# Performance work log

Hardware: AMD Instinct MI355X
Metric: run time of the kernel (lower is better)

The kernel has to match this reference:

```python
import jax, jax.numpy as jnp
import numpy as np

N, H, E, K, C, M = 4096, 512, 512, 64, 128, 4  # tokens, hidden, embed, categories, children/cat, max_num_children
IN = E + H  # LSTMCell input size


def setup_inputs() -> dict:
    key = jax.random.key(0)
    ks = jax.random.split(key, 12)
    s = 0.05
    return {
        "et": jax.random.normal(ks[0], (N, H), jnp.float32),
        "x": jax.random.normal(ks[1], (N, IN), jnp.float32),
        "h": jax.random.normal(ks[2], (N, H), jnp.float32),
        "c": jax.random.normal(ks[3], (N, H), jnp.float32),
        "cat": jax.random.randint(ks[4], (N,), 0, K, jnp.int32),
        "ci": jax.random.randint(ks[5], (N,), 0, M, jnp.int32),
        # per-category prediction Linear(hidden_size -> |children(category)|)
        "W_lin": jax.random.normal(ks[6], (K, C, H), jnp.float32) * s,
        "b_lin": jax.random.normal(ks[7], (K, C), jnp.float32) * s,
        # per-child-index LSTMCell(embedding+hidden -> hidden), torch gate order i,f,g,o
        "W_ih": jax.random.normal(ks[8], (M, 4 * H, IN), jnp.float32) * s,
        "W_hh": jax.random.normal(ks[9], (M, 4 * H, H), jnp.float32) * s,
        "b_ih": jax.random.normal(ks[10], (M, 4 * H), jnp.float32) * s,
        "b_hh": jax.random.normal(ks[11], (M, 4 * H), jnp.float32) * s,
    }


def reference(et, x, h, c, cat, ci, W_lin, b_lin, W_ih, W_hh, b_ih, b_hh):
    # get_log_odds: route each token to its category's Linear (gather weights, per-token matvec)
    Wg = W_lin[cat]                                   # [N, C, H]
    log_odds = jnp.einsum('nh,nch->nc', et, Wg) + b_lin[cat]  # [N, C]

    # get_next: LSTMCell selected by child_index. Only M=4 cells, so compute all
    # cells' gates densely (efficient GEMMs) and select with a one-hot mix.
    gates_all = (jnp.einsum('ni,kgi->nkg', x, W_ih)
                 + jnp.einsum('nh,kgh->nkg', h, W_hh)
                 + (b_ih + b_hh)[None])               # [N, M, 4H]
    sel = jax.nn.one_hot(ci, M, dtype=gates_all.dtype)  # [N, M]
    gates = jnp.einsum('nkg,nk->ng', gates_all, sel)     # [N, 4H]
    i_, f_, g_, o_ = jnp.split(gates, 4, axis=-1)
    c2 = jax.nn.sigmoid(f_) * c + jax.nn.sigmoid(i_) * jnp.tanh(g_)
    h2 = jax.nn.sigmoid(o_) * jnp.tanh(c2)
    return log_odds, h2, c2
```

## Files before the change

kernel.cpp:

```cpp
#include <hip/hip_runtime.h>
#include <hip/hip_bf16.h>
#include <stdint.h>

#define NTOK 4096
#define HID  512
#define INSZ 1024
#define KIN  1536
#define KCAT 64
#define CCH  128
#define MCELL 4
#define G4H  2048
#define SLOTS 4992

typedef unsigned short u16;
typedef __bf16 bf16x8 __attribute__((ext_vector_type(8)));
typedef float  f32x4  __attribute__((ext_vector_type(4)));

__device__ __forceinline__ u16 f2bf(float f) {
    unsigned u = __float_as_uint(f);
    u += 0x7fffu + ((u >> 16) & 1u);
    return (u16)(u >> 16);
}
__device__ __forceinline__ float bf2f(u16 v) {
    return __uint_as_float(((unsigned)v) << 16);
}
__device__ __forceinline__ void store_bf8(u16* p, float4 a, float4 b) {
    ushort4 r0, r1;
    r0.x = f2bf(a.x); r0.y = f2bf(a.y); r0.z = f2bf(a.z); r0.w = f2bf(a.w);
    r1.x = f2bf(b.x); r1.y = f2bf(b.y); r1.z = f2bf(b.z); r1.w = f2bf(b.w);
    *reinterpret_cast<ushort4*>(p) = r0;
    *reinterpret_cast<ushort4*>(p + 4) = r1;
}
__device__ __forceinline__ void gl16(const u16* g, u16* l) {
    __builtin_amdgcn_global_load_lds((const __attribute__((address_space(1))) void*)g,
                                     (__attribute__((address_space(3))) void*)l, 16, 0, 0);
}

#define CH_W  (8192 * 192)
#define CH_L  (8192 * 64)
#define CH_A  (4097 * 192)
#define CH_TOT (CH_W + CH_L + CH_A)
#define PK_BLOCKS 2048

__global__ __launch_bounds__(256) void fat_pack(
    const float* __restrict__ x, const float* __restrict__ h,
    const float* __restrict__ Wih, const float* __restrict__ Whh,
    const float* __restrict__ W_lin,
    const int* __restrict__ ci, const int* __restrict__ cat,
    int* __restrict__ meta, int* __restrict__ perm_ci, int* __restrict__ perm_cat,
    u16* __restrict__ A_tok, u16* __restrict__ Wb, u16* __restrict__ Wlin)
{
    if (blockIdx.x == 0) {
        __shared__ int cnt_ci[MCELL], cur_ci[MCELL];
        __shared__ int cnt_cat[KCAT], cur_cat[KCAT];
        __shared__ int scan_cat[KCAT];
        int tid = threadIdx.x;
        if (tid < MCELL) cnt_ci[tid] = 0;
        if (tid < KCAT)  cnt_cat[tid] = 0;
        __syncthreads();
        for (int t = tid; t < NTOK; t += 256) {
            atomicAdd(&cnt_ci[ci[t]], 1);
            atomicAdd(&cnt_cat[cat[t]], 1);
        }
        __syncthreads();
        for (int i = tid; i < 128; i += 256) meta[136 + i] = -1;
        if (tid < MCELL) {
            int off = 0;
            for (int i = 0; i < tid; ++i) off += (cnt_ci[i] + 191) / 192 * 192;
            int p = (cnt_ci[tid] + 191) / 192 * 192;
            meta[tid] = p; meta[4 + tid] = off; cur_ci[tid] = off;
        }
        if (tid < KCAT) scan_cat[tid] = (cnt_cat[tid] + 63) & ~63;
        __syncthreads();
        for (int d = 1; d < KCAT; d <<= 1) {
            int v = 0;
            if (tid < KCAT && tid >= d) v = scan_cat[tid - d];
            __syncthreads();
            if (tid < KCAT) scan_cat[tid] += v;
            __syncthreads();
        }
        if (tid < KCAT) {
            int p = (cnt_cat[tid] + 63) & ~63;
            int off = scan_cat[tid] - p;
            meta[8 + tid] = p; meta[72 + tid] = off; cur_cat[tid] = off;
            for (int i = 0; i < p / 64; ++i) meta[136 + off / 64 + i] = tid;
        }
        __syncthreads();
        for (int i = tid; i < SLOTS; i += 256) perm_ci[i] = -1;
        for (int i = tid; i < 8192; i += 256) perm_cat[i] = -1;
        __syncthreads();
        for (int t = tid; t < NTOK; t += 256) {
            perm_ci[atomicAdd(&cur_ci[ci[t]], 1)] = t;
            perm_cat[atomicAdd(&cur_cat[cat[t]], 1)] = t;
        }
        return;
    }
    for (int i = (blockIdx.x - 1) * 256 + threadIdx.x; i < CH_TOT; i += (PK_BLOCKS - 1) * 256) {
        if (i < CH_W) {
            int row = i / 192, cc = i - row * 192;
            int m = row >> 11, j = row & 2047;
            int srow = (j & 3) * HID + (j >> 2);
            int c = cc * 8;
            const float* src = (c < INSZ) ? (Wih + ((size_t)m * G4H + srow) * INSZ + c)
                                          : (Whh + ((size_t)m * G4H + srow) * HID + (c - INSZ));
            store_bf8(Wb + (size_t)row * KIN + c,
                      *(const float4*)src, *(const float4*)(src + 4));
        } else if (i < CH_W + CH_L) {
            int i2 = i - CH_W;
            int row = i2 >> 6, cc = i2 & 63;
            const float* src = W_lin + (size_t)row * HID + cc * 8;
            store_bf8(Wlin + (size_t)row * HID + cc * 8,
                      *(const float4*)src, *(const float4*)(src + 4));
        } else {
            int i3 = i - (CH_W + CH_L);
            int row = i3 / 192, cc = i3 - row * 192;
            int c = cc * 8;
            u16* dst = A_tok + (size_t)row * KIN + c;
            if (row == NTOK) {
                *reinterpret_cast<int4*>(dst) = make_int4(0, 0, 0, 0);
            } else {
                const float* src = (c < INSZ) ? (x + (size_t)row * INSZ + c)
                                              : (h + (size_t)row * HID + (c - INSZ));
                store_bf8(dst, *(const float4*)src, *(const float4*)(src + 4));
            }
        }
    }
}

__global__ __launch_bounds__(256, 3) void mega_gemm(
    const u16* __restrict__ A_tok,
    const u16* __restrict__ Wb,
    const u16* __restrict__ Wlin,
    const float* __restrict__ et,
    const float* __restrict__ b_lin,
    const float* __restrict__ c,
    const float* __restrict__ b_ih,
    const float* __restrict__ b_hh,
    const int* __restrict__ meta,
    const int* __restrict__ perm_ci,
    const int* __restrict__ perm_cat,
    float* __restrict__ out)
{
    __shared__ __align__(16) u16 S[20480];
    __shared__ int sperm[192];

    int tid = threadIdx.x;
    int lane = tid & 63, wave = tid >> 6;
    int qd = lane >> 4, l15 = lane & 15;
    int rsw = l15 & 7;

    int id = blockIdx.x;
    if (id < 1408) {
        int g = id & 63;
        int rt = id >> 6;
        int m = g >> 4, ct = g & 15;
        int pcnt = meta[m];
        if (rt * 192 >= pcnt) return;
        int row0 = meta[4 + m] + rt * 192;

        if (tid < 192) sperm[tid] = perm_ci[row0 + tid];
        __syncthreads();

        const u16* gA[6]; const u16* gB[4];
        u16* lA[6]; u16* lB[4];
        #pragma unroll
        for (int j = 0; j < 6; ++j) {
            int q = j * 256 + tid;
            int row = q >> 3, kc = (q & 7) ^ (row & 7);
            int t = sperm[row];
            gA[j] = A_tok + (size_t)(t >= 0 ? t : NTOK) * KIN + kc * 8;
            lA[j] = &S[q * 8];
        }
        #pragma unroll
        for (int j = 0; j < 4; ++j) {
            int q = j * 256 + tid;
            int row = q >> 3, kc = (q & 7) ^ (row & 7);
            gB[j] = Wb + ((size_t)m * G4H + ct * 128 + row) * KIN + kc * 8;
            lB[j] = &S[12288 + q * 8];
        }

        int wm = wave >> 1, wn = wave & 1;

        f32x4 acc[6][4];
        #pragma unroll
        for (int i = 0; i < 6; ++i)
            #pragma unroll
            for (int j = 0; j < 4; ++j)
                acc[i][j] = (f32x4){0.f, 0.f, 0.f, 0.f};

        for (int ks = 0; ks < KIN / 64; ++ks) {
            #pragma unroll
            for (int j = 0; j < 6; ++j) { gl16(gA[j], lA[j]); gA[j] += 64; }
            #pragma unroll
            for (int j = 0; j < 4; ++j) { gl16(gB[j], lB[j]); gB[j] += 64; }
            __syncthreads();
            #pragma unroll
            for (int ks2 = 0; ks2 < 2; ++ks2) {
                int ch = (ks2 * 4 + qd) ^ rsw;
                bf16x8 fb[4];
                #pragma unroll
                for (int tj = 0; tj < 4; ++tj) {
                    int row = wn * 64 + tj * 16 + l15;
                    fb[tj] = *reinterpret_cast<const bf16x8*>(&S[12288 + row * 64 + ch * 8]);
                }
                #pragma unroll
                for (int ti = 0; ti < 6; ++ti) {
                    int row = wm * 96 + ti * 16 + l15;
                    bf16x8 fa = *reinterpret_cast<const bf16x8*>(&S[row * 64 + ch * 8]);
                    #pragma unroll
                    for (int tj = 0; tj < 4; ++tj)
                        acc[ti][tj] = __builtin_amdgcn_mfma_f32_16x16x32_bf16(fa, fb[tj], acc[ti][tj], 0, 0, 0);
                }
            }
            __syncthreads();
        }

        int gt = l15 & 3;
        float bias[4];
        #pragma unroll
        for (int tj = 0; tj < 4; ++tj) {
            int u = ct * 32 + wn * 16 + tj * 4 + (l15 >> 2);
            bias[tj] = b_ih[m * G4H + gt * HID + u] + b_hh[m * G4H + gt * HID + u];
        }
        int b0 = lane & 1, b1 = lane & 2;
        const size_t o_h2 = (size_t)NTOK * CCH;
        const size_t o_c2 = o_h2 + (size_t)NTOK * HID;
        #pragma unroll
        for (int ti = 0; ti < 6; ++ti) {
            int t = sperm[wm * 96 + ti * 16 + qd * 4 + (lane & 3)];
            #pragma unroll
            for (int tj = 0; tj < 4; ++tj) {
                float v0 = acc[ti][tj][0] + bias[tj];
                float v1 = acc[ti][tj][1] + bias[tj];
                float v2 = acc[ti][tj][2] + bias[tj];
                float v3 = acc[ti][tj][3] + bias[tj];
                float tmp;
                tmp = __shfl_xor(b0 ? v0 : v1, 1); if (b0) v0 = tmp; else v1 = tmp;
                tmp = __shfl_xor(b0 ? v2 : v3, 1); if (b0) v2 = tmp; else v3 = tmp;
                tmp = __shfl_xor(b1 ? v0 : v2, 2); if (b1) v0 = tmp; else v2 = tmp;
                tmp = __shfl_xor(b1 ? v1 : v3, 2); if (b1) v1 = tmp; else v3 = tmp;
                if (t >= 0) {
                    int u = ct * 32 + wn * 16 + tj * 4 + (l15 >> 2);
                    float si = 1.f / (1.f + __expf(-v0));
                    float sf = 1.f / (1.f + __expf(-v1));
                    float tg = tanhf(v2);
                    float so = 1.f / (1.f + __expf(-v3));
                    float cold = c[(size_t)t * HID + u];
                    float c2 = sf * cold + si * tg;
                    float h2 = so * tanhf(c2);
                    out[o_h2 + (size_t)t * HID + u] = h2;
                    out[o_c2 + (size_t)t * HID + u] = c2;
                }
            }
        }
    } else {
        u16* As = S;
        u16* Bs = S + 8192;
        int rtl = id - 1408;
        int k = meta[136 + rtl];
        if (k < 0) return;
        int r0 = rtl * 64;

        if (tid < 64) sperm[tid] = perm_cat[r0 + tid];
        __syncthreads();

        int rb = tid >> 3;
        int kc = (tid & 7) ^ (rb & 7);

        const u16* gW[4]; u16* lW[4];
        #pragma unroll
        for (int i = 0; i < 4; ++i) {
            gW[i] = Wlin + ((size_t)k * CCH + i * 32 + rb) * HID + kc * 8;
            lW[i] = As + (i * 256 + wave * 64) * 8;
        }
        int ar = tid >> 2;
        int acp = tid & 3;
        int at = sperm[ar];
        const float* asrc = (at >= 0) ? (et + (size_t)at * HID) : nullptr;

        f32x4 acc[4][2];
        #pragma unroll
        for (int i = 0; i < 4; ++i) {
            acc[i][0] = (f32x4){0.f, 0.f, 0.f, 0.f};
            acc[i][1] = (f32x4){0.f, 0.f, 0.f, 0.f};
        }

        for (int kk = 0; kk < HID; kk += 64) {
            #pragma unroll
            for (int i = 0; i < 4; ++i) { gl16(gW[i], lW[i]); gW[i] += 64; }
            #pragma unroll
            for (int j = 0; j < 2; ++j) {
                int dch = acp * 2 + j;
                int sch = dch ^ (ar & 7);
                u16* dst = &Bs[ar * 64 + dch * 8];
                if (asrc) {
                    const float* s = asrc + kk + sch * 8;
                    store_bf8(dst, *(const float4*)s, *(const float4*)(s + 4));
                } else {
                    *reinterpret_cast<int4*>(dst) = make_int4(0, 0, 0, 0);
                }
            }
            __syncthreads();
            #pragma unroll
            for (int ks2 = 0; ks2 < 2; ++ks2) {
                int ch = (ks2 * 4 + qd) ^ rsw;
                bf16x8 fa[4], fb[2];
                #pragma unroll
                for (int ti = 0; ti < 4; ++ti)
                    fa[ti] = *reinterpret_cast<const bf16x8*>(&Bs[(ti * 16 + l15) * 64 + ch * 8]);
                #pragma unroll
                for (int tj = 0; tj < 2; ++tj)
                    fb[tj] = *reinterpret_cast<const bf16x8*>(&As[(wave * 32 + tj * 16 + l15) * 64 + ch * 8]);
                #pragma unroll
                for (int ti = 0; ti < 4; ++ti)
                    #pragma unroll
                    for (int tj = 0; tj < 2; ++tj)
                        acc[ti][tj] = __builtin_amdgcn_mfma_f32_16x16x32_bf16(fa[ti], fb[tj], acc[ti][tj], 0, 0, 0);
            }
            __syncthreads();
        }

        #pragma unroll
        for (int ti = 0; ti < 4; ++ti) {
            #pragma unroll
            for (int tj = 0; tj < 2; ++tj) {
                int n = wave * 32 + tj * 16 + l15;
                float bias = b_lin[k * CCH + n];
                #pragma unroll
                for (int rr = 0; rr < 4; ++rr) {
                    int row = ti * 16 + qd * 4 + rr;
                    int t = sperm[row];
                    if (t >= 0)
                        out[(size_t)t * CCH + n] = acc[ti][tj][rr] + bias;
                }
            }
        }
    }
}

extern "C" void kernel_launch(void* const* d_in, const int* in_sizes, int n_in,
                              void* d_out, int out_size, void* d_ws, size_t ws_size,
                              hipStream_t stream) {
    const float* et    = (const float*)d_in[0];
    const float* x     = (const float*)d_in[1];
    const float* h     = (const float*)d_in[2];
    const float* c     = (const float*)d_in[3];
    const int*   cat   = (const int*)d_in[4];
    const int*   ci    = (const int*)d_in[5];
    const float* W_lin = (const float*)d_in[6];
    const float* b_lin = (const float*)d_in[7];
    const float* W_ih  = (const float*)d_in[8];
    const float* W_hh  = (const float*)d_in[9];
    const float* b_ih  = (const float*)d_in[10];
    const float* b_hh  = (const float*)d_in[11];
    float* out = (float*)d_out;

    char* ws = (char*)d_ws;
    int* meta     = (int*)ws;
    int* perm_ci  = (int*)(ws + 2048);
    int* perm_cat = (int*)(ws + 22528);
    u16* A_tok    = (u16*)(ws + 55296);
    u16* Wb       = (u16*)(ws + 12641280);
    u16* Wlin     = (u16*)(ws + 37807104);

    fat_pack<<<PK_BLOCKS, 256, 0, stream>>>(x, h, W_ih, W_hh, W_lin, ci, cat,
                                            meta, perm_ci, perm_cat, A_tok, Wb, Wlin);

    mega_gemm<<<1408 + 128, 256, 0, stream>>>(A_tok, Wb, Wlin, et, b_lin, c,
                                              b_ih, b_hh, meta, perm_ci, perm_cat, out);
}
```

Before: 220.7 us.

## Widen LSTM GEMM tiles to 512 threads and convert W_lin inline

```diff
diff --git a/kernel.cpp b/kernel.cpp
--- a/kernel.cpp
+++ b/kernel.cpp
@@ -37,18 +37,16 @@
 }
 
 #define CH_W  (8192 * 192)
-#define CH_L  (8192 * 64)
 #define CH_A  (4097 * 192)
-#define CH_TOT (CH_W + CH_L + CH_A)
+#define CH_TOT (CH_W + CH_A)
 #define PK_BLOCKS 2048
 
 __global__ __launch_bounds__(256) void fat_pack(
     const float* __restrict__ x, const float* __restrict__ h,
     const float* __restrict__ Wih, const float* __restrict__ Whh,
-    const float* __restrict__ W_lin,
     const int* __restrict__ ci, const int* __restrict__ cat,
     int* __restrict__ meta, int* __restrict__ perm_ci, int* __restrict__ perm_cat,
-    u16* __restrict__ A_tok, u16* __restrict__ Wb, u16* __restrict__ Wlin)
+    u16* __restrict__ A_tok, u16* __restrict__ Wb)
 {
     if (blockIdx.x == 0) {
         __shared__ int cnt_ci[MCELL], cur_ci[MCELL];
@@ -105,14 +103,8 @@
                                           : (Whh + ((size_t)m * G4H + srow) * HID + (c - INSZ));
             store_bf8(Wb + (size_t)row * KIN + c,
                       *(const float4*)src, *(const float4*)(src + 4));
-        } else if (i < CH_W + CH_L) {
-            int i2 = i - CH_W;
-            int row = i2 >> 6, cc = i2 & 63;
-            const float* src = W_lin + (size_t)row * HID + cc * 8;
-            store_bf8(Wlin + (size_t)row * HID + cc * 8,
-                      *(const float4*)src, *(const float4*)(src + 4));
         } else {
-            int i3 = i - (CH_W + CH_L);
+            int i3 = i - CH_W;
             int row = i3 / 192, cc = i3 - row * 192;
             int c = cc * 8;
             u16* dst = A_tok + (size_t)row * KIN + c;
@@ -127,10 +119,10 @@
     }
 }
 
-__global__ __launch_bounds__(256, 3) void mega_gemm(
+__global__ __launch_bounds__(512, 2) void mega_gemm(
     const u16* __restrict__ A_tok,
     const u16* __restrict__ Wb,
-    const u16* __restrict__ Wlin,
+    const float* __restrict__ W_lin,
     const float* __restrict__ et,
     const float* __restrict__ b_lin,
     const float* __restrict__ c,
@@ -141,19 +133,18 @@
     const int* __restrict__ perm_cat,
     float* __restrict__ out)
 {
-    __shared__ __align__(16) u16 S[20480];
+    __shared__ __align__(16) u16 S[28672];
     __shared__ int sperm[192];
 
     int tid = threadIdx.x;
-    int lane = tid & 63, wave = tid >> 6;
+    int lane = tid & 63;
     int qd = lane >> 4, l15 = lane & 15;
     int rsw = l15 & 7;
 
     int id = blockIdx.x;
-    if (id < 1408) {
-        int g = id & 63;
-        int rt = id >> 6;
-        int m = g >> 4, ct = g & 15;
+    if (id < 704) {
+        int g = id & 31, rt = id >> 5;
+        int m = g >> 3, ct = g & 7;
         int pcnt = meta[m];
         if (rt * 192 >= pcnt) return;
         int row0 = meta[4 + m] + rt * 192;
@@ -161,25 +152,26 @@
         if (tid < 192) sperm[tid] = perm_ci[row0 + tid];
         __syncthreads();
 
-        const u16* gA[6]; const u16* gB[4];
-        u16* lA[6]; u16* lB[4];
-        #pragma unroll
-        for (int j = 0; j < 6; ++j) {
-            int q = j * 256 + tid;
+        const u16* gA[3]; u16* lA[3];
+        #pragma unroll
+        for (int j = 0; j < 3; ++j) {
+            int q = j * 512 + tid;
             int row = q >> 3, kc = (q & 7) ^ (row & 7);
             int t = sperm[row];
             gA[j] = A_tok + (size_t)(t >= 0 ? t : NTOK) * KIN + kc * 8;
             lA[j] = &S[q * 8];
         }
+        const u16* gB[4]; u16* lB[4];
         #pragma unroll
         for (int j = 0; j < 4; ++j) {
-            int q = j * 256 + tid;
+            int q = j * 512 + tid;
             int row = q >> 3, kc = (q & 7) ^ (row & 7);
-            gB[j] = Wb + ((size_t)m * G4H + ct * 128 + row) * KIN + kc * 8;
+            gB[j] = Wb + ((size_t)m * G4H + ct * 256 + row) * KIN + kc * 8;
             lB[j] = &S[12288 + q * 8];
         }
 
-        int wm = wave >> 1, wn = wave & 1;
+        int wave = tid >> 6;
+        int wm = wave >> 2, wn = wave & 3;
 
         f32x4 acc[6][4];
         #pragma unroll
@@ -190,7 +182,7 @@
 
         for (int ks = 0; ks < KIN / 64; ++ks) {
             #pragma unroll
-            for (int j = 0; j < 6; ++j) { gl16(gA[j], lA[j]); gA[j] += 64; }
+            for (int j = 0; j < 3; ++j) { gl16(gA[j], lA[j]); gA[j] += 64; }
             #pragma unroll
             for (int j = 0; j < 4; ++j) { gl16(gB[j], lB[j]); gB[j] += 64; }
             __syncthreads();
@@ -219,7 +211,7 @@
         float bias[4];
         #pragma unroll
         for (int tj = 0; tj < 4; ++tj) {
-            int u = ct * 32 + wn * 16 + tj * 4 + (l15 >> 2);
+            int u = ct * 64 + wn * 16 + tj * 4 + (l15 >> 2);
             bias[tj] = b_ih[m * G4H + gt * HID + u] + b_hh[m * G4H + gt * HID + u];
         }
         int b0 = lane & 1, b1 = lane & 2;
@@ -240,7 +232,7 @@
                 tmp = __shfl_xor(b1 ? v0 : v2, 2); if (b1) v0 = tmp; else v2 = tmp;
                 tmp = __shfl_xor(b1 ? v1 : v3, 2); if (b1) v1 = tmp; else v3 = tmp;
                 if (t >= 0) {
-                    int u = ct * 32 + wn * 16 + tj * 4 + (l15 >> 2);
+                    int u = ct * 64 + wn * 16 + tj * 4 + (l15 >> 2);
                     float si = 1.f / (1.f + __expf(-v0));
                     float sf = 1.f / (1.f + __expf(-v1));
                     float tg = tanhf(v2);
@@ -254,28 +246,34 @@
             }
         }
     } else {
-        u16* As = S;
-        u16* Bs = S + 8192;
-        int rtl = id - 1408;
+        int half = tid >> 8;
+        int tid2 = tid & 255;
+        int wave2 = tid2 >> 6;
+        u16* As = S + half * 12288;
+        u16* Bs = As + 8192;
+        int* sp = sperm + half * 64;
+
+        int rtl = (id - 704) * 2 + half;
         int k = meta[136 + rtl];
-        if (k < 0) return;
+        int valid = (k >= 0);
+        if (!valid) k = 0;
         int r0 = rtl * 64;
 
-        if (tid < 64) sperm[tid] = perm_cat[r0 + tid];
-        __syncthreads();
-
-        int rb = tid >> 3;
-        int kc = (tid & 7) ^ (rb & 7);
-
-        const u16* gW[4]; u16* lW[4];
+        if (tid2 < 64) sp[tid2] = valid ? perm_cat[r0 + tid2] : -1;
+        __syncthreads();
+
+        int rb = tid2 >> 3;
+        int wkc = (tid2 & 7) ^ (rb & 7);
+
+        const float* wsrc[4]; u16* wdst[4];
         #pragma unroll
         for (int i = 0; i < 4; ++i) {
-            gW[i] = Wlin + ((size_t)k * CCH + i * 32 + rb) * HID + kc * 8;
-            lW[i] = As + (i * 256 + wave * 64) * 8;
-        }
-        int ar = tid >> 2;
-        int acp = tid & 3;
-        int at = sperm[ar];
+            wsrc[i] = W_lin + ((size_t)k * CCH + i * 32 + rb) * HID + wkc * 8;
+            wdst[i] = As + ((size_t)i * 256 + tid2) * 8;
+        }
+        int ar = tid2 >> 2;
+        int acp = tid2 & 3;
+        int at = sp[ar];
         const float* asrc = (at >= 0) ? (et + (size_t)at * HID) : nullptr;
 
         f32x4 acc[4][2];
@@ -287,7 +285,10 @@
 
         for (int kk = 0; kk < HID; kk += 64) {
             #pragma unroll
-            for (int i = 0; i < 4; ++i) { gl16(gW[i], lW[i]); gW[i] += 64; }
+            for (int i = 0; i < 4; ++i) {
+                const float* s = wsrc[i] + kk;
+                store_bf8(wdst[i], *(const float4*)s, *(const float4*)(s + 4));
+            }
             #pragma unroll
             for (int j = 0; j < 2; ++j) {
                 int dch = acp * 2 + j;
@@ -310,7 +311,7 @@
                     fa[ti] = *reinterpret_cast<const bf16x8*>(&Bs[(ti * 16 + l15) * 64 + ch * 8]);
                 #pragma unroll
                 for (int tj = 0; tj < 2; ++tj)
-                    fb[tj] = *reinterpret_cast<const bf16x8*>(&As[(wave * 32 + tj * 16 + l15) * 64 + ch * 8]);
+                    fb[tj] = *reinterpret_cast<const bf16x8*>(&As[(wave2 * 32 + tj * 16 + l15) * 64 + ch * 8]);
                 #pragma unroll
                 for (int ti = 0; ti < 4; ++ti)
                     #pragma unroll
@@ -324,12 +325,12 @@
         for (int ti = 0; ti < 4; ++ti) {
             #pragma unroll
             for (int tj = 0; tj < 2; ++tj) {
-                int n = wave * 32 + tj * 16 + l15;
+                int n = wave2 * 32 + tj * 16 + l15;
                 float bias = b_lin[k * CCH + n];
                 #pragma unroll
                 for (int rr = 0; rr < 4; ++rr) {
                     int row = ti * 16 + qd * 4 + rr;
-                    int t = sperm[row];
+                    int t = sp[row];
                     if (t >= 0)
                         out[(size_t)t * CCH + n] = acc[ti][tj][rr] + bias;
                 }
@@ -361,11 +362,10 @@
     int* perm_cat = (int*)(ws + 22528);
     u16* A_tok    = (u16*)(ws + 55296);
     u16* Wb       = (u16*)(ws + 12641280);
-    u16* Wlin     = (u16*)(ws + 37807104);
-
-    fat_pack<<<PK_BLOCKS, 256, 0, stream>>>(x, h, W_ih, W_hh, W_lin, ci, cat,
-                                            meta, perm_ci, perm_cat, A_tok, Wb, Wlin);
-
-    mega_gemm<<<1408 + 128, 256, 0, stream>>>(A_tok, Wb, Wlin, et, b_lin, c,
-                                              b_ih, b_hh, meta, perm_ci, perm_cat, out);
-}
+
+    fat_pack<<<PK_BLOCKS, 256, 0, stream>>>(x, h, W_ih, W_hh, ci, cat,
+                                            meta, perm_ci, perm_cat, A_tok, Wb);
+
+    mega_gemm<<<704 + 64, 512, 0, stream>>>(A_tok, Wb, W_lin, et, b_lin, c,
+                                            b_ih, b_hh, meta, perm_ci, perm_cat, out);
+}
```

Result: no change. 221.5 us (+0.4%).

## Shrink LSTM GEMM tiles to 128 rows, convert W_lin in-kernel, fast activations

Applied to the files above, without the earlier changes.

```diff
diff --git a/kernel.cpp b/kernel.cpp
--- a/kernel.cpp
+++ b/kernel.cpp
@@ -10,7 +10,7 @@
 #define CCH  128
 #define MCELL 4
 #define G4H  2048
-#define SLOTS 4992
+#define SLOTS 4608
 
 typedef unsigned short u16;
 typedef __bf16 bf16x8 __attribute__((ext_vector_type(8)));
@@ -35,20 +35,25 @@
     __builtin_amdgcn_global_load_lds((const __attribute__((address_space(1))) void*)g,
                                      (__attribute__((address_space(3))) void*)l, 16, 0, 0);
 }
+__device__ __forceinline__ float fsig(float x) {
+    return __builtin_amdgcn_rcpf(1.f + __expf(-x));
+}
+__device__ __forceinline__ float ftanh(float x) {
+    float e2 = __expf(fminf(2.f * x, 20.f));
+    return (e2 - 1.f) * __builtin_amdgcn_rcpf(e2 + 1.f);
+}
 
 #define CH_W  (8192 * 192)
-#define CH_L  (8192 * 64)
 #define CH_A  (4097 * 192)
-#define CH_TOT (CH_W + CH_L + CH_A)
+#define CH_TOT (CH_W + CH_A)
 #define PK_BLOCKS 2048
 
 __global__ __launch_bounds__(256) void fat_pack(
     const float* __restrict__ x, const float* __restrict__ h,
     const float* __restrict__ Wih, const float* __restrict__ Whh,
-    const float* __restrict__ W_lin,
     const int* __restrict__ ci, const int* __restrict__ cat,
     int* __restrict__ meta, int* __restrict__ perm_ci, int* __restrict__ perm_cat,
-    u16* __restrict__ A_tok, u16* __restrict__ Wb, u16* __restrict__ Wlin)
+    u16* __restrict__ A_tok, u16* __restrict__ Wb)
 {
     if (blockIdx.x == 0) {
         __shared__ int cnt_ci[MCELL], cur_ci[MCELL];
@@ -66,8 +71,8 @@
         for (int i = tid; i < 128; i += 256) meta[136 + i] = -1;
         if (tid < MCELL) {
             int off = 0;
-            for (int i = 0; i < tid; ++i) off += (cnt_ci[i] + 191) / 192 * 192;
-            int p = (cnt_ci[tid] + 191) / 192 * 192;
+            for (int i = 0; i < tid; ++i) off += (cnt_ci[i] + 127) & ~127;
+            int p = (cnt_ci[tid] + 127) & ~127;
             meta[tid] = p; meta[4 + tid] = off; cur_ci[tid] = off;
         }
         if (tid < KCAT) scan_cat[tid] = (cnt_cat[tid] + 63) & ~63;
@@ -105,14 +110,8 @@
                                           : (Whh + ((size_t)m * G4H + srow) * HID + (c - INSZ));
             store_bf8(Wb + (size_t)row * KIN + c,
                       *(const float4*)src, *(const float4*)(src + 4));
-        } else if (i < CH_W + CH_L) {
-            int i2 = i - CH_W;
-            int row = i2 >> 6, cc = i2 & 63;
-            const float* src = W_lin + (size_t)row * HID + cc * 8;
-            store_bf8(Wlin + (size_t)row * HID + cc * 8,
-                      *(const float4*)src, *(const float4*)(src + 4));
         } else {
-            int i3 = i - (CH_W + CH_L);
+            int i3 = i - CH_W;
             int row = i3 / 192, cc = i3 - row * 192;
             int c = cc * 8;
             u16* dst = A_tok + (size_t)row * KIN + c;
@@ -127,10 +126,10 @@
     }
 }
 
-__global__ __launch_bounds__(256, 3) void mega_gemm(
+__global__ __launch_bounds__(256, 4) void mega_gemm(
     const u16* __restrict__ A_tok,
     const u16* __restrict__ Wb,
-    const u16* __restrict__ Wlin,
+    const float* __restrict__ W_lin,
     const float* __restrict__ et,
     const float* __restrict__ b_lin,
     const float* __restrict__ c,
@@ -141,8 +140,7 @@
     const int* __restrict__ perm_cat,
     float* __restrict__ out)
 {
-    __shared__ __align__(16) u16 S[20480];
-    __shared__ int sperm[192];
+    __shared__ __align__(16) u16 S[16384];
 
     int tid = threadIdx.x;
     int lane = tid & 63, wave = tid >> 6;
@@ -150,49 +148,43 @@
     int rsw = l15 & 7;
 
     int id = blockIdx.x;
-    if (id < 1408) {
+    if (id < 2048) {
         int g = id & 63;
         int rt = id >> 6;
         int m = g >> 4, ct = g & 15;
         int pcnt = meta[m];
-        if (rt * 192 >= pcnt) return;
-        int row0 = meta[4 + m] + rt * 192;
-
-        if (tid < 192) sperm[tid] = perm_ci[row0 + tid];
-        __syncthreads();
-
-        const u16* gA[6]; const u16* gB[4];
-        u16* lA[6]; u16* lB[4];
-        #pragma unroll
-        for (int j = 0; j < 6; ++j) {
-            int q = j * 256 + tid;
-            int row = q >> 3, kc = (q & 7) ^ (row & 7);
-            int t = sperm[row];
-            gA[j] = A_tok + (size_t)(t >= 0 ? t : NTOK) * KIN + kc * 8;
-            lA[j] = &S[q * 8];
-        }
+        if (rt * 128 >= pcnt) return;
+        int row0 = meta[4 + m] + rt * 128;
+
+        const u16* gA[4]; const u16* gB[4];
+        int qq[4];
         #pragma unroll
         for (int j = 0; j < 4; ++j) {
             int q = j * 256 + tid;
             int row = q >> 3, kc = (q & 7) ^ (row & 7);
+            int t = perm_ci[row0 + row];
+            gA[j] = A_tok + (size_t)(t >= 0 ? t : NTOK) * KIN + kc * 8;
             gB[j] = Wb + ((size_t)m * G4H + ct * 128 + row) * KIN + kc * 8;
-            lB[j] = &S[12288 + q * 8];
-        }
-
+            qq[j] = q * 8;
+        }
         int wm = wave >> 1, wn = wave & 1;
-
-        f32x4 acc[6][4];
-        #pragma unroll
-        for (int i = 0; i < 6; ++i)
+        int trow[4];
+        #pragma unroll
+        for (int ti = 0; ti < 4; ++ti)
+            trow[ti] = perm_ci[row0 + wm * 64 + ti * 16 + qd * 4 + (lane & 3)];
+
+        f32x4 acc[4][4];
+        #pragma unroll
+        for (int i = 0; i < 4; ++i)
             #pragma unroll
             for (int j = 0; j < 4; ++j)
                 acc[i][j] = (f32x4){0.f, 0.f, 0.f, 0.f};
 
         for (int ks = 0; ks < KIN / 64; ++ks) {
             #pragma unroll
-            for (int j = 0; j < 6; ++j) { gl16(gA[j], lA[j]); gA[j] += 64; }
-            #pragma unroll
-            for (int j = 0; j < 4; ++j) { gl16(gB[j], lB[j]); gB[j] += 64; }
+            for (int j = 0; j < 4; ++j) { gl16(gA[j], &S[qq[j]]); gA[j] += 64; }
+            #pragma unroll
+            for (int j = 0; j < 4; ++j) { gl16(gB[j], &S[8192 + qq[j]]); gB[j] += 64; }
             __syncthreads();
             #pragma unroll
             for (int ks2 = 0; ks2 < 2; ++ks2) {
@@ -201,11 +193,11 @@
                 #pragma unroll
                 for (int tj = 0; tj < 4; ++tj) {
                     int row = wn * 64 + tj * 16 + l15;
-                    fb[tj] = *reinterpret_cast<const bf16x8*>(&S[12288 + row * 64 + ch * 8]);
-                }
-                #pragma unroll
-                for (int ti = 0; ti < 6; ++ti) {
-                    int row = wm * 96 + ti * 16 + l15;
+                    fb[tj] = *reinterpret_cast<const bf16x8*>(&S[8192 + row * 64 + ch * 8]);
+                }
+                #pragma unroll
+                for (int ti = 0; ti < 4; ++ti) {
+                    int row = wm * 64 + ti * 16 + l15;
                     bf16x8 fa = *reinterpret_cast<const bf16x8*>(&S[row * 64 + ch * 8]);
                     #pragma unroll
                     for (int tj = 0; tj < 4; ++tj)
@@ -226,8 +218,8 @@
         const size_t o_h2 = (size_t)NTOK * CCH;
         const size_t o_c2 = o_h2 + (size_t)NTOK * HID;
         #pragma unroll
-        for (int ti = 0; ti < 6; ++ti) {
-            int t = sperm[wm * 96 + ti * 16 + qd * 4 + (lane & 3)];
+        for (int ti = 0; ti < 4; ++ti) {
+            int t = trow[ti];
             #pragma unroll
             for (int tj = 0; tj < 4; ++tj) {
                 float v0 = acc[ti][tj][0] + bias[tj];
@@ -241,13 +233,13 @@
                 tmp = __shfl_xor(b1 ? v1 : v3, 2); if (b1) v1 = tmp; else v3 = tmp;
                 if (t >= 0) {
                     int u = ct * 32 + wn * 16 + tj * 4 + (l15 >> 2);
-                    float si = 1.f / (1.f + __expf(-v0));
-                    float sf = 1.f / (1.f + __expf(-v1));
-                    float tg = tanhf(v2);
-                    float so = 1.f / (1.f + __expf(-v3));
+                    float si = fsig(v0);
+                    float sf = fsig(v1);
+                    float tg = ftanh(v2);
+                    float so = fsig(v3);
                     float cold = c[(size_t)t * HID + u];
                     float c2 = sf * cold + si * tg;
-                    float h2 = so * tanhf(c2);
+                    float h2 = so * ftanh(c2);
                     out[o_h2 + (size_t)t * HID + u] = h2;
                     out[o_c2 + (size_t)t * HID + u] = c2;
                 }
@@ -256,26 +248,24 @@
     } else {
         u16* As = S;
         u16* Bs = S + 8192;
-        int rtl = id - 1408;
+        int rtl = id - 2048;
         int k = meta[136 + rtl];
-        if (k < 0) return;
+        int valid = (k >= 0);
+        if (!valid) return;
         int r0 = rtl * 64;
 
-        if (tid < 64) sperm[tid] = perm_cat[r0 + tid];
-        __syncthreads();
-
         int rb = tid >> 3;
-        int kc = (tid & 7) ^ (rb & 7);
-
-        const u16* gW[4]; u16* lW[4];
+        int wkc = (tid & 7) ^ (rb & 7);
+
+        const float* wsrc[4]; u16* wdst[4];
         #pragma unroll
         for (int i = 0; i < 4; ++i) {
-            gW[i] = Wlin + ((size_t)k * CCH + i * 32 + rb) * HID + kc * 8;
-            lW[i] = As + (i * 256 + wave * 64) * 8;
+            wsrc[i] = W_lin + ((size_t)k * CCH + i * 32 + rb) * HID + wkc * 8;
+            wdst[i] = As + ((size_t)i * 256 + tid) * 8;
         }
         int ar = tid >> 2;
         int acp = tid & 3;
-        int at = sperm[ar];
+        int at = perm_cat[r0 + ar];
         const float* asrc = (at >= 0) ? (et + (size_t)at * HID) : nullptr;
 
         f32x4 acc[4][2];
@@ -287,7 +277,10 @@
 
         for (int kk = 0; kk < HID; kk += 64) {
             #pragma unroll
-            for (int i = 0; i < 4; ++i) { gl16(gW[i], lW[i]); gW[i] += 64; }
+            for (int i = 0; i < 4; ++i) {
+                const float* s = wsrc[i] + kk;
+                store_bf8(wdst[i], *(const float4*)s, *(const float4*)(s + 4));
+            }
             #pragma unroll
             for (int j = 0; j < 2; ++j) {
                 int dch = acp * 2 + j;
@@ -329,7 +322,7 @@
                 #pragma unroll
                 for (int rr = 0; rr < 4; ++rr) {
                     int row = ti * 16 + qd * 4 + rr;
-                    int t = sperm[row];
+                    int t = perm_cat[r0 + row];
                     if (t >= 0)
                         out[(size_t)t * CCH + n] = acc[ti][tj][rr] + bias;
                 }
@@ -361,11 +354,10 @@
     int* perm_cat = (int*)(ws + 22528);
     u16* A_tok    = (u16*)(ws + 55296);
     u16* Wb       = (u16*)(ws + 12641280);
-    u16* Wlin     = (u16*)(ws + 37807104);
-
-    fat_pack<<<PK_BLOCKS, 256, 0, stream>>>(x, h, W_ih, W_hh, W_lin, ci, cat,
-                                            meta, perm_ci, perm_cat, A_tok, Wb, Wlin);
-
-    mega_gemm<<<1408 + 128, 256, 0, stream>>>(A_tok, Wb, Wlin, et, b_lin, c,
+
+    fat_pack<<<PK_BLOCKS, 256, 0, stream>>>(x, h, W_ih, W_hh, ci, cat,
+                                            meta, perm_ci, perm_cat, A_tok, Wb);
+
+    mega_gemm<<<2048 + 128, 256, 0, stream>>>(A_tok, Wb, W_lin, et, b_lin, c,
                                               b_ih, b_hh, meta, perm_ci, perm_cat, out);
 }
```

Result: slower. 248.9 us (+12.8%).
